# Kernel optimization log

Measured on AMD Instinct MI355X. Metric: run time of the kernel, lower is better.

The kernel has to match this reference:

```python
import jax, jax.numpy as jnp
import numpy as np

N = 50000        # n_nodes
E = 1_600_000    # n_edges (before self-loops)
D_IN, HID, HEADS, D_OUT = 32, 64, 4, 32
NEG_SLOPE = 0.2  # PyG GATConv default leaky_relu slope


def setup_inputs() -> dict:
    key = jax.random.key(0)
    ks = jax.random.split(key, 10)
    x = jax.random.normal(ks[0], (N, D_IN), jnp.float32)
    edge_index = jax.random.randint(ks[1], (2, E), 0, N, dtype=jnp.int64)
    s = 0.1
    W_gcn = jax.random.normal(ks[2], (D_IN, HID), jnp.float32) * s
    b_gcn = jnp.zeros((HID,), jnp.float32)
    W_gat = jax.random.normal(ks[3], (HID, HEADS * HID), jnp.float32) * s
    att_src = jax.random.normal(ks[4], (HEADS, HID), jnp.float32) * s
    att_dst = jax.random.normal(ks[5], (HEADS, HID), jnp.float32) * s
    b_gat = jnp.zeros((HEADS * HID,), jnp.float32)
    W_fc = jax.random.normal(ks[6], (HEADS * HID, D_OUT), jnp.float32) * s
    b_fc = jnp.zeros((D_OUT,), jnp.float32)
    return dict(x=x, edge_index=edge_index, W_gcn=W_gcn, b_gcn=b_gcn,
                W_gat=W_gat, att_src=att_src, att_dst=att_dst, b_gat=b_gat,
                W_fc=W_fc, b_fc=b_fc)


def _add_self_loops(edge_index, n):
    loop = jnp.arange(n, dtype=edge_index.dtype)
    src = jnp.concatenate([edge_index[0], loop])
    dst = jnp.concatenate([edge_index[1], loop])
    return src, dst


def _gcn(x, src, dst, W, b):
    h = x @ W                                               # (N, HID)
    deg = jax.ops.segment_sum(jnp.ones_like(src, jnp.float32), dst, N)
    dinv = jnp.where(deg > 0, jax.lax.rsqrt(deg), 0.0)
    norm = dinv[src] * dinv[dst]                            # (E+N,)
    out = jax.ops.segment_sum(h[src] * norm[:, None], dst, N)
    return out + b


def _gat(x, src, dst, W, att_src, att_dst, b):
    h = (x @ W).reshape(N, HEADS, HID)                      # (N, H, C)
    a_s = jnp.einsum('nhc,hc->nh', h, att_src)              # (N, H)
    a_d = jnp.einsum('nhc,hc->nh', h, att_dst)
    e = jax.nn.leaky_relu(a_s[src] + a_d[dst], NEG_SLOPE)   # (E+N, H)
    # softmax over incoming edges per destination node
    m = jax.ops.segment_max(e, dst, N)                      # every dst has a self-loop
    w = jnp.exp(e - m[dst])
    denom = jax.ops.segment_sum(w, dst, N)
    alpha = w / denom[dst]                                  # (E+N, H)
    out = jax.ops.segment_sum(h[src] * alpha[:, :, None], dst, N)
    return out.reshape(N, HEADS * HID) + b


def reference(x, edge_index, W_gcn, b_gcn, W_gat, att_src, att_dst, b_gat, W_fc, b_fc):
    src, dst = _add_self_loops(edge_index, N)
    h = jax.nn.relu(_gcn(x, src, dst, W_gcn, b_gcn))        # dropout: eval mode (identity)
    h = jax.nn.relu(_gat(h, src, dst, W_gat, att_src, att_dst, b_gat))
    return h @ W_fc + b_fc
```

## Files before the change

### kernel.cpp

```cpp
#include <hip/hip_runtime.h>
#include <hip/hip_bf16.h>
#include <hip/hip_fp16.h>
#include <math.h>

#define N_NODES 50000
#define N_EDGES 1600000
#define D_IN    32
#define HID     64
#define HEADS   4
#define D_OUT   32
#define NEG_SLOPE 0.2f
#define NTILES 3125

#define CQ 64

#define NBKT 196
#define NBLK_A 391
#define TILE_A 4096
#define GH (NBKT * NBLK_A)
#define NSB 300
#define CAP 10240

typedef _Float16 half8 __attribute__((ext_vector_type(8)));
typedef float    f32x4 __attribute__((ext_vector_type(4)));
typedef float    f32x2 __attribute__((ext_vector_type(2)));

__global__ __launch_bounds__(256) void histA(const int* __restrict__ edge,
                                             int* __restrict__ ghist) {
    __shared__ int hist[4][NBKT];
    int t = threadIdx.x, wv = t >> 6;
    for (int i = t; i < 4 * NBKT; i += 256) ((int*)hist)[i] = 0;
    __syncthreads();
    int base = blockIdx.x * TILE_A;
#pragma unroll
    for (int k = 0; k < 16; k++) {
        int i = base + k * 256 + t;
        if (i < N_EDGES) atomicAdd(&hist[wv][edge[N_EDGES + i] >> 8], 1);
    }
    __syncthreads();
    for (int b = t; b < NBKT; b += 256)
        ghist[b * NBLK_A + blockIdx.x] = hist[0][b] + hist[1][b] + hist[2][b] + hist[3][b];
}

__global__ __launch_bounds__(256) void scanB1(const int* __restrict__ g,
                                              int* __restrict__ bsum) {
    int t = threadIdx.x;
    int i = blockIdx.x * 256 + t;
    int v = (i < GH) ? g[i] : 0;
#pragma unroll
    for (int off = 32; off; off >>= 1) v += __shfl_xor(v, off);
    __shared__ int ws[4];
    if ((t & 63) == 0) ws[t >> 6] = v;
    __syncthreads();
    if (t == 0) bsum[blockIdx.x] = ws[0] + ws[1] + ws[2] + ws[3];
}

__global__ __launch_bounds__(320) void scanB2_attvec(int* __restrict__ bsum,
                                                     const float* __restrict__ W,
                                                     const float* __restrict__ att_s,
                                                     const float* __restrict__ att_d,
                                                     float* __restrict__ vsrc,
                                                     float* __restrict__ vdst) {
    int t = threadIdx.x, lane = t & 63, wv = t >> 6;
    if (blockIdx.x == 0) {
        int v = (t < NSB) ? bsum[t] : 0;
        int inc = v;
#pragma unroll
        for (int d = 1; d < 64; d <<= 1) {
            int u = __shfl_up(inc, d);
            if (lane >= d) inc += u;
        }
        __shared__ int ws[5];
        if (lane == 63) ws[wv] = inc;
        __syncthreads();
        int add = 0;
#pragma unroll
        for (int j = 0; j < 5; j++) if (j < wv) add += ws[j];
        if (t < NSB) bsum[t] = add + inc - v;
    } else if (t < 256) {
        int h = t >> 6, k = t & 63;
        float s_ = 0.f, d_ = 0.f;
#pragma unroll 8
        for (int c = 0; c < 64; c++) {
            float w = W[k * 256 + h * 64 + c];
            s_ += w * att_s[h * 64 + c];
            d_ += w * att_d[h * 64 + c];
        }
        vsrc[h * 64 + k] = s_;
        vdst[h * 64 + k] = d_;
    }
}

__global__ __launch_bounds__(256) void scanB3(int* __restrict__ g,
                                              const int* __restrict__ bsum) {
    int t = threadIdx.x, lane = t & 63, wv = t >> 6;
    int i = blockIdx.x * 256 + t;
    int v = (i < GH) ? g[i] : 0;
    int inc = v;
#pragma unroll
    for (int d = 1; d < 64; d <<= 1) {
        int u = __shfl_up(inc, d);
        if (lane >= d) inc += u;
    }
    __shared__ int ws[4];
    if (lane == 63) ws[wv] = inc;
    __syncthreads();
    int add = 0;
#pragma unroll
    for (int j = 0; j < 4; j++) if (j < wv) add += ws[j];
    if (i < GH) g[i] = bsum[blockIdx.x] + add + inc - v;
}

__global__ __launch_bounds__(256) void scatterC(const int* __restrict__ edge,
                                                const int* __restrict__ ghist,
                                                unsigned* __restrict__ tmp) {
    __shared__ int cur[NBKT];
    int t = threadIdx.x;
    if (t < NBKT) cur[t] = ghist[t * NBLK_A + blockIdx.x];
    __syncthreads();
    int base = blockIdx.x * TILE_A;
#pragma unroll
    for (int k = 0; k < 16; k++) {
        int i = base + k * 256 + t;
        if (i < N_EDGES) {
            int s = edge[i], d = edge[N_EDGES + i];
            int pos = atomicAdd(&cur[d >> 8], 1);
            tmp[pos] = ((unsigned)d << 16) | (unsigned)s;
        }
    }
}

__global__ __launch_bounds__(256) void sortD(const unsigned* __restrict__ tmp,
                                             const int* __restrict__ ghist,
                                             unsigned short* __restrict__ colidx,
                                             int* __restrict__ rowptr,
                                             float* __restrict__ dinv) {
    __shared__ unsigned char  dl8[CAP];
    __shared__ unsigned short s16[CAP];
    __shared__ unsigned short o16[CAP];
    __shared__ int hist[4][256];
    __shared__ int excl[256];
    __shared__ int wsum[4];
    int t = threadIdx.x, lane = t & 63, wv = t >> 6;
    int b = blockIdx.x;
    int lo = ghist[b * NBLK_A];
    int hi = (b < NBKT - 1) ? ghist[(b + 1) * NBLK_A] : N_EDGES;
    int size = hi - lo;
    if (size > CAP) size = CAP;
    for (int i = t; i < 4 * 256; i += 256) ((int*)hist)[i] = 0;
    __syncthreads();
    for (int i = t; i < size; i += 256) {
        unsigned key = tmp[lo + i];
        int dl = (key >> 16) & 255;
        dl8[i] = (unsigned char)dl;
        s16[i] = (unsigned short)(key & 0xFFFF);
        atomicAdd(&hist[wv][dl], 1);
    }
    __syncthreads();
    int h = hist[0][t] + hist[1][t] + hist[2][t] + hist[3][t];
    int inc = h;
#pragma unroll
    for (int d = 1; d < 64; d <<= 1) {
        int u = __shfl_up(inc, d);
        if (lane >= d) inc += u;
    }
    if (lane == 63) wsum[wv] = inc;
    __syncthreads();
    int add = 0;
#pragma unroll
    for (int j = 0; j < 4; j++) if (j < wv) add += wsum[j];
    int ex = inc - h + add;
    excl[t] = ex;
    int node = b * 256 + t;
    if (node < N_NODES) {
        rowptr[node] = lo + ex;
        dinv[node]   = rsqrtf((float)(h + 1));
    }
    if (b == NBKT - 1 && t == 0) rowptr[N_NODES] = N_EDGES;
    __syncthreads();
    for (int i = t; i < size; i += 256) {
        int pos = atomicAdd(&excl[dl8[i]], 1);
        o16[pos] = s16[i];
    }
    __syncthreads();
    for (int i = t; i < size; i += 256) colidx[lo + i] = o16[i];
}

__global__ __launch_bounds__(256) void gemm1(const float* __restrict__ x,
                                             const float* __restrict__ W,
                                             const float* __restrict__ dinv,
                                             __half* __restrict__ h,
                                             __half* __restrict__ h1) {
    __shared__ float Wl[D_IN * HID];
    int t = threadIdx.x;
    if (blockIdx.x == 0 && t < HID) {
        h [(size_t)N_NODES * HID + t] = __float2half(0.f);
        h1[(size_t)N_NODES * HID + t] = __float2half(0.f);
    }
    for (int i = t; i < D_IN * HID; i += 256) Wl[i] = W[i];
    __syncthreads();
    int c = t & 63, rw = t >> 6;
    int r0 = blockIdx.x * 32;
#pragma unroll
    for (int rr = 0; rr < 8; rr++) {
        int r = r0 + rr * 4 + rw;
        if (r >= N_NODES) break;
        const float4* xr4 = (const float4*)(x + r * D_IN);
        float acc = 0.f;
#pragma unroll
        for (int k4 = 0; k4 < D_IN / 4; k4++) {
            float4 xv = xr4[k4];
            int k = k4 * 4;
            acc += xv.x * Wl[(k+0)*HID + c] + xv.y * Wl[(k+1)*HID + c]
                 + xv.z * Wl[(k+2)*HID + c] + xv.w * Wl[(k+3)*HID + c];
        }
        h[r * HID + c] = __float2half(acc * dinv[r]);
    }
}

__global__ __launch_bounds__(256, 8) void gcn_agg(const __half* __restrict__ h,
                                               const int* __restrict__ rowptr,
                                               const unsigned short* __restrict__ colidx,
                                               const float* __restrict__ dinv,
                                               const float* __restrict__ b,
                                               const float* __restrict__ vsrc,
                                               const float* __restrict__ vdst,
                                               __half* __restrict__ h1,
                                               float* __restrict__ as_o,
                                               float* __restrict__ ad_o) {
    __shared__ int sbuf[4][4][CQ + 1];
    int lane = threadIdx.x & 63, wv = threadIdx.x >> 6;
    int quarter = lane >> 4, ql = lane & 15;
    int n = blockIdx.x * 16 + wv * 4 + quarter;
    int rp = rowptr[n], re = rowptr[n + 1];
    int deg = re - rp;
    int dm = deg;
    dm = max(dm, __shfl_xor(dm, 16));
    dm = max(dm, __shfl_xor(dm, 32));
    f32x2 a01 = {0.f, 0.f}, a23 = {0.f, 0.f};
    const __half* hp = h + ql * 4;
    int* sq = sbuf[wv][quarter];
    for (int cb = 0; cb < dm; cb += CQ) {
        int m  = min(CQ, max(deg - cb, 0));
        int mm = min(CQ, dm - cb);
        int mm8 = (mm + 7) & ~7;
        for (int j = ql; j < m; j += 16)
            sq[j] = (int)colidx[rp + cb + j] * HID;
        for (int j = m + ql; j < mm8; j += 16)
            sq[j] = N_NODES * HID;
        for (int i0 = 0; i0 < mm8; i0 += 8) {
            float2 raw[8];
#pragma unroll
            for (int k = 0; k < 8; k++)
                raw[k] = *(const float2*)(hp + sq[i0 + k]);
#pragma unroll
            for (int k = 0; k < 8; k++) {
                __half2 g0 = __builtin_bit_cast(__half2, raw[k].x);
                __half2 g1 = __builtin_bit_cast(__half2, raw[k].y);
                float2 f0 = __half22float2(g0), f1 = __half22float2(g1);
                a01.x += f0.x; a01.y += f0.y;
                a23.x += f1.x; a23.y += f1.y;
            }
        }
    }
    {
        float2 raw = *(const float2*)(hp + n * HID);
        __half2 g0 = __builtin_bit_cast(__half2, raw.x);
        __half2 g1 = __builtin_bit_cast(__half2, raw.y);
        float2 f0 = __half22float2(g0), f1 = __half22float2(g1);
        a01.x += f0.x; a01.y += f0.y;
        a23.x += f1.x; a23.y += f1.y;
    }
    float dn = dinv[n];
    const float4 bb = *(const float4*)&b[ql * 4];
    float v0 = fmaxf(a01.x * dn + bb.x, 0.f);
    float v1 = fmaxf(a01.y * dn + bb.y, 0.f);
    float v2 = fmaxf(a23.x * dn + bb.z, 0.f);
    float v3 = fmaxf(a23.y * dn + bb.w, 0.f);
    __half2* op = (__half2*)&h1[n * HID + ql * 4];
    op[0] = __floats2half2_rn(v0, v1);
    op[1] = __floats2half2_rn(v2, v3);
#pragma unroll
    for (int hh = 0; hh < 4; hh++) {
        float4 vsp = *(const float4*)&vsrc[hh * 64 + ql * 4];
        float4 vdp = *(const float4*)&vdst[hh * 64 + ql * 4];
        float vs = v0 * vsp.x + v1 * vsp.y + v2 * vsp.z + v3 * vsp.w;
        float vd = v0 * vdp.x + v1 * vdp.y + v2 * vdp.z + v3 * vdp.w;
#pragma unroll
        for (int off = 8; off > 0; off >>= 1) {
            vs += __shfl_xor(vs, off);
            vd += __shfl_xor(vd, off);
        }
        if (ql == 0) {
            as_o[n * 4 + hh] = vs;
            ad_o[n * 4 + hh] = vd;
        }
    }
}

__global__ __launch_bounds__(256, 8) void gat_agg(const __half* __restrict__ h1,
                                               const int* __restrict__ rowptr,
                                               const unsigned short* __restrict__ colidx,
                                               const float* __restrict__ a_s,
                                               const float* __restrict__ a_d,
                                               __half* __restrict__ u) {
    __shared__ float4 wbuf[4][4][CQ + 1];
    __shared__ int    sbuf[4][4][CQ + 1];
    int lane = threadIdx.x & 63, wv = threadIdx.x >> 6;
    int quarter = lane >> 4, ql = lane & 15;
    int n = blockIdx.x * 16 + wv * 4 + quarter;
    int rp = rowptr[n], re = rowptr[n + 1];
    int deg = re - rp;
    int dm = deg;
    dm = max(dm, __shfl_xor(dm, 16));
    dm = max(dm, __shfl_xor(dm, 32));
    float4 ad4 = *(const float4*)&a_d[n * 4];

    float dnx = 0.f, dny = 0.f, dnz = 0.f, dnw = 0.f;
    f32x2 acc[4][2];
#pragma unroll
    for (int hh = 0; hh < 4; hh++) { acc[hh][0] = (f32x2){0.f,0.f}; acc[hh][1] = (f32x2){0.f,0.f}; }
    const __half* hp = h1 + ql * 4;
    int*    sq = sbuf[wv][quarter];
    float4* wq = wbuf[wv][quarter];
    for (int cb = 0; cb < dm; cb += CQ) {
        int m  = min(CQ, max(deg - cb, 0));
        int mm = min(CQ, dm - cb);
        int mm8 = (mm + 7) & ~7;
        for (int j = ql; j < m; j += 16) {
            int s = colidx[rp + cb + j];
            float4 a = *(const float4*)&a_s[s * 4];
            float vx = a.x + ad4.x; vx = fmaxf(vx, NEG_SLOPE * vx);
            float vy = a.y + ad4.y; vy = fmaxf(vy, NEG_SLOPE * vy);
            float vz = a.z + ad4.z; vz = fmaxf(vz, NEG_SLOPE * vz);
            float vw = a.w + ad4.w; vw = fmaxf(vw, NEG_SLOPE * vw);
            float wx = __expf(vx), wy = __expf(vy);
            float wz = __expf(vz), ww = __expf(vw);
            dnx += wx; dny += wy; dnz += wz; dnw += ww;
            sq[j] = s * HID;
            wq[j] = make_float4(wx, wy, wz, ww);
        }
        for (int j = m + ql; j < mm8; j += 16) {
            sq[j] = N_NODES * HID;
            wq[j] = make_float4(0.f, 0.f, 0.f, 0.f);
        }
        for (int i0 = 0; i0 < mm8; i0 += 8) {
            float2 raw[8];
#pragma unroll
            for (int k = 0; k < 8; k++)
                raw[k] = *(const float2*)(hp + sq[i0 + k]);
#pragma unroll
            for (int k = 0; k < 8; k++) {
                float4 w4 = wq[i0 + k];
                __half2 g0 = __builtin_bit_cast(__half2, raw[k].x);
                __half2 g1 = __builtin_bit_cast(__half2, raw[k].y);
                float2 t0 = __half22float2(g0), t1 = __half22float2(g1);
                f32x2 f0 = {t0.x, t0.y}, f1 = {t1.x, t1.y};
                f32x2 wx2 = {w4.x, w4.x}, wy2 = {w4.y, w4.y};
                f32x2 wz2 = {w4.z, w4.z}, ww2 = {w4.w, w4.w};
                acc[0][0] += wx2 * f0; acc[0][1] += wx2 * f1;
                acc[1][0] += wy2 * f0; acc[1][1] += wy2 * f1;
                acc[2][0] += wz2 * f0; acc[2][1] += wz2 * f1;
                acc[3][0] += ww2 * f0; acc[3][1] += ww2 * f1;
            }
        }
    }
#pragma unroll
    for (int off = 8; off > 0; off >>= 1) {
        dnx += __shfl_xor(dnx, off);
        dny += __shfl_xor(dny, off);
        dnz += __shfl_xor(dnz, off);
        dnw += __shfl_xor(dnw, off);
    }
    float4 asn = *(const float4*)&a_s[n * 4];
    float sx = asn.x + ad4.x; sx = fmaxf(sx, NEG_SLOPE * sx);
    float sy = asn.y + ad4.y; sy = fmaxf(sy, NEG_SLOPE * sy);
    float sz = asn.z + ad4.z; sz = fmaxf(sz, NEG_SLOPE * sz);
    float sw = asn.w + ad4.w; sw = fmaxf(sw, NEG_SLOPE * sw);
    float wsx = __expf(sx), wsy = __expf(sy);
    float wsz = __expf(sz), wsw = __expf(sw);
    dnx += wsx; dny += wsy; dnz += wsz; dnw += wsw;
    {
        float2 raw = *(const float2*)(hp + n * HID);
        __half2 g0 = __builtin_bit_cast(__half2, raw.x);
        __half2 g1 = __builtin_bit_cast(__half2, raw.y);
        float2 t0 = __half22float2(g0), t1 = __half22float2(g1);
        acc[0][0].x += wsx * t0.x; acc[0][0].y += wsx * t0.y; acc[0][1].x += wsx * t1.x; acc[0][1].y += wsx * t1.y;
        acc[1][0].x += wsy * t0.x; acc[1][0].y += wsy * t0.y; acc[1][1].x += wsy * t1.x; acc[1][1].y += wsy * t1.y;
        acc[2][0].x += wsz * t0.x; acc[2][0].y += wsz * t0.y; acc[2][1].x += wsz * t1.x; acc[2][1].y += wsz * t1.y;
        acc[3][0].x += wsw * t0.x; acc[3][0].y += wsw * t0.y; acc[3][1].x += wsw * t1.x; acc[3][1].y += wsw * t1.y;
    }
    float r4[4] = {1.f / dnx, 1.f / dny, 1.f / dnz, 1.f / dnw};
    __half* up = u + n * 256 + ql * 4;
#pragma unroll
    for (int hh = 0; hh < 4; hh++) {
        __half2* op = (__half2*)&up[hh * 64];
        op[0] = __floats2half2_rn(acc[hh][0].x * r4[hh], acc[hh][0].y * r4[hh]);
        op[1] = __floats2half2_rn(acc[hh][1].x * r4[hh], acc[hh][1].y * r4[hh]);
    }
}

__global__ __launch_bounds__(256) void gemm2b(const __half* __restrict__ u,
                                              const float* __restrict__ W,
                                              const float* __restrict__ b,
                                              __half* __restrict__ h2) {
    int lane = threadIdx.x & 63, hd = threadIdx.x >> 6;
    int quad = lane >> 4, l16 = lane & 15;
    half8 Bf[4][2];
#pragma unroll
    for (int nt = 0; nt < 4; nt++)
#pragma unroll
        for (int kc = 0; kc < 2; kc++) {
            const float* wp = W + (kc * 32 + quad * 8) * 256 + hd * 64 + nt * 16 + l16;
#pragma unroll
            for (int j = 0; j < 8; j++)
                Bf[nt][kc][j] = (_Float16)wp[j * 256];
        }
    float bb[4];
#pragma unroll
    for (int nt = 0; nt < 4; nt++) bb[nt] = b[hd * 64 + nt * 16 + l16];

    int rt0 = blockIdx.x * 5;
#pragma unroll
    for (int i = 0; i < 5; i++) {
        int rt = rt0 + i;
        const __half* up = u + ((size_t)(rt * 16 + l16)) * 256 + hd * 64 + quad * 8;
        half8 A0 = *(const half8*)(const void*)up;
        half8 A1 = *(const half8*)(const void*)(up + 32);
        f32x4 acc[4];
#pragma unroll
        for (int nt = 0; nt < 4; nt++) {
            acc[nt] = (f32x4){0.f, 0.f, 0.f, 0.f};
            acc[nt] = __builtin_amdgcn_mfma_f32_16x16x32_f16(A0, Bf[nt][0], acc[nt], 0, 0, 0);
            acc[nt] = __builtin_amdgcn_mfma_f32_16x16x32_f16(A1, Bf[nt][1], acc[nt], 0, 0, 0);
        }
#pragma unroll
        for (int nt = 0; nt < 4; nt++) {
            int col = hd * 64 + nt * 16 + l16;
#pragma unroll
            for (int reg = 0; reg < 4; reg++) {
                int row = rt * 16 + quad * 4 + reg;
                h2[(size_t)row * 256 + col] = __float2half(fmaxf(acc[nt][reg] + bb[nt], 0.f));
            }
        }
    }
}

__global__ __launch_bounds__(256) void gemm3(const __half* __restrict__ h2,
                                             const float* __restrict__ W,
                                             const float* __restrict__ b,
                                             float* __restrict__ out) {
    int lane = threadIdx.x & 63, wv = threadIdx.x >> 6;
    int quad = lane >> 4, l16 = lane & 15;
    half8 Bf[2][8];
#pragma unroll
    for (int nt = 0; nt < 2; nt++)
#pragma unroll
        for (int kc = 0; kc < 8; kc++) {
            const float* wp = W + (kc * 32 + quad * 8) * 32 + nt * 16 + l16;
#pragma unroll
            for (int j = 0; j < 8; j++)
                Bf[nt][kc][j] = (_Float16)wp[j * 32];
        }
    float bb0 = b[l16], bb1 = b[16 + l16];

    for (int tile = blockIdx.x * 4 + wv; tile < NTILES; tile += gridDim.x * 4) {
        const __half* hp = h2 + (size_t)(tile * 16 + l16) * 256 + quad * 8;
        f32x4 acc0 = {0.f, 0.f, 0.f, 0.f};
        f32x4 acc1 = {0.f, 0.f, 0.f, 0.f};
#pragma unroll
        for (int kc = 0; kc < 8; kc++) {
            half8 A = *(const half8*)(const void*)(hp + kc * 32);
            acc0 = __builtin_amdgcn_mfma_f32_16x16x32_f16(A, Bf[0][kc], acc0, 0, 0, 0);
            acc1 = __builtin_amdgcn_mfma_f32_16x16x32_f16(A, Bf[1][kc], acc1, 0, 0, 0);
        }
#pragma unroll
        for (int reg = 0; reg < 4; reg++) {
            int row = tile * 16 + quad * 4 + reg;
            out[row * 32 + l16]      = acc0[reg] + bb0;
            out[row * 32 + 16 + l16] = acc1[reg] + bb1;
        }
    }
}

extern "C" void kernel_launch(void* const* d_in, const int* in_sizes, int n_in,
                              void* d_out, int out_size, void* d_ws, size_t ws_size,
                              hipStream_t stream) {
    const float* x      = (const float*)d_in[0];
    const int*   edge   = (const int*)  d_in[1];
    const float* W_gcn  = (const float*)d_in[2];
    const float* b_gcn  = (const float*)d_in[3];
    const float* W_gat  = (const float*)d_in[4];
    const float* att_s  = (const float*)d_in[5];
    const float* att_d  = (const float*)d_in[6];
    const float* b_gat  = (const float*)d_in[7];
    const float* W_fc   = (const float*)d_in[8];
    const float* b_fc   = (const float*)d_in[9];
    float* out = (float*)d_out;

    char* p = (char*)d_ws;
    auto alloc = [&](size_t bytes) {
        char* q = p;
        p += (bytes + 255) & ~(size_t)255;
        return q;
    };
    __half* h     = (__half*)alloc((size_t)(N_NODES + 1) * HID * 2);
    __half* h1    = (__half*)alloc((size_t)(N_NODES + 1) * HID * 2);
    __half* u     = (__half*)alloc((size_t)N_NODES * 256 * 2);
    __half* h2    = (__half*)alloc((size_t)N_NODES * 256 * 2);
    float* as_a   = (float*)alloc((size_t)N_NODES * 4 * 4);
    float* ad_a   = (float*)alloc((size_t)N_NODES * 4 * 4);
    float* dinv   = (float*)alloc((size_t)N_NODES * 4);
    int*   rowptr = (int*)  alloc((size_t)(N_NODES + 1) * 4);
    unsigned short* colidx = (unsigned short*)alloc((size_t)N_EDGES * 2);
    int*   ghist  = (int*)  alloc((size_t)GH * 4);
    int*   bsum   = (int*)  alloc((size_t)NSB * 4);
    unsigned* tmp = (unsigned*)alloc((size_t)N_EDGES * 4);
    float* vsrc   = (float*)alloc((size_t)HEADS * HID * 4);
    float* vdst   = (float*)alloc((size_t)HEADS * HID * 4);

    histA        <<<NBLK_A, 256, 0, stream>>>(edge, ghist);
    scanB1       <<<NSB, 256, 0, stream>>>(ghist, bsum);
    scanB2_attvec<<<2, 320, 0, stream>>>(bsum, W_gat, att_s, att_d, vsrc, vdst);
    scanB3       <<<NSB, 256, 0, stream>>>(ghist, bsum);
    scatterC     <<<NBLK_A, 256, 0, stream>>>(edge, ghist, tmp);
    sortD        <<<NBKT, 256, 0, stream>>>(tmp, ghist, colidx, rowptr, dinv);

    gemm1   <<<(N_NODES + 31) / 32, 256, 0, stream>>>(x, W_gcn, dinv, h, h1);
    gcn_agg <<<(N_NODES + 15) / 16, 256, 0, stream>>>(h, rowptr, colidx, dinv, b_gcn,
                                                      vsrc, vdst, h1, as_a, ad_a);

    gat_agg <<<(N_NODES + 15) / 16, 256, 0, stream>>>(h1, rowptr, colidx, as_a, ad_a, u);
    gemm2b  <<<625, 256, 0, stream>>>(u, W_gat, b_gat, h2);

    gemm3   <<<256, 256, 0, stream>>>(h2, W_fc, b_fc, out);
}
```

Baseline: 227.7 us.

## Process 8 nodes per wavefront with 16-byte gathers in GCN/GAT aggregation

Both aggregation kernels now assign 8 lanes per destination node instead of 16, so each lane gathers 8 fp16 features with a single 16-byte load, and each block covers 32 nodes. Bounds guards are added because 50000 is not a multiple of 32. The GAT neighbor chunk size is cut to 32 to keep shared memory in check, and the occupancy hint in launch_bounds is removed. This halves the number of gather instructions per edge and widens each load, at the cost of more registers per lane and more divergence across the 8 nodes in a wavefront.

```diff
diff --git a/kernel.cpp b/kernel.cpp
--- a/kernel.cpp
+++ b/kernel.cpp
@@ -12,7 +12,8 @@
 #define NEG_SLOPE 0.2f
 #define NTILES 3125
 
-#define CQ 64
+#define CQG 64
+#define CQA 32
 
 #define NBKT 196
 #define NBLK_A 391
@@ -218,7 +219,7 @@
     }
 }
 
-__global__ __launch_bounds__(256, 8) void gcn_agg(const __half* __restrict__ h,
+__global__ __launch_bounds__(256) void gcn_agg(const __half* __restrict__ h,
                                                const int* __restrict__ rowptr,
                                                const unsigned short* __restrict__ colidx,
                                                const float* __restrict__ dinv,
@@ -228,106 +229,134 @@
                                                __half* __restrict__ h1,
                                                float* __restrict__ as_o,
                                                float* __restrict__ ad_o) {
-    __shared__ int sbuf[4][4][CQ + 1];
+    __shared__ int sbuf[4][8][CQG + 1];
     int lane = threadIdx.x & 63, wv = threadIdx.x >> 6;
-    int quarter = lane >> 4, ql = lane & 15;
-    int n = blockIdx.x * 16 + wv * 4 + quarter;
-    int rp = rowptr[n], re = rowptr[n + 1];
-    int deg = re - rp;
+    int oct = lane >> 3, ol = lane & 7;
+    int n = blockIdx.x * 32 + wv * 8 + oct;
+    int nn = min(n, N_NODES - 1);
+    int rp = rowptr[nn], re = rowptr[nn + 1];
+    int deg = (n < N_NODES) ? (re - rp) : 0;
     int dm = deg;
+    dm = max(dm, __shfl_xor(dm, 8));
     dm = max(dm, __shfl_xor(dm, 16));
     dm = max(dm, __shfl_xor(dm, 32));
-    f32x2 a01 = {0.f, 0.f}, a23 = {0.f, 0.f};
-    const __half* hp = h + ql * 4;
-    int* sq = sbuf[wv][quarter];
-    for (int cb = 0; cb < dm; cb += CQ) {
-        int m  = min(CQ, max(deg - cb, 0));
-        int mm = min(CQ, dm - cb);
+    f32x4 a0 = {0.f,0.f,0.f,0.f}, a1 = {0.f,0.f,0.f,0.f};
+    const __half* hp = h + ol * 8;
+    int* sq = sbuf[wv][oct];
+    for (int cb = 0; cb < dm; cb += CQG) {
+        int m  = min(CQG, max(deg - cb, 0));
+        int mm = min(CQG, dm - cb);
         int mm8 = (mm + 7) & ~7;
-        for (int j = ql; j < m; j += 16)
+        for (int j = ol; j < m; j += 8)
             sq[j] = (int)colidx[rp + cb + j] * HID;
-        for (int j = m + ql; j < mm8; j += 16)
+        for (int j = m + ol; j < mm8; j += 8)
             sq[j] = N_NODES * HID;
         for (int i0 = 0; i0 < mm8; i0 += 8) {
-            float2 raw[8];
+            float4 raw[8];
 #pragma unroll
             for (int k = 0; k < 8; k++)
-                raw[k] = *(const float2*)(hp + sq[i0 + k]);
+                raw[k] = *(const float4*)(hp + sq[i0 + k]);
 #pragma unroll
             for (int k = 0; k < 8; k++) {
                 __half2 g0 = __builtin_bit_cast(__half2, raw[k].x);
                 __half2 g1 = __builtin_bit_cast(__half2, raw[k].y);
+                __half2 g2 = __builtin_bit_cast(__half2, raw[k].z);
+                __half2 g3 = __builtin_bit_cast(__half2, raw[k].w);
                 float2 f0 = __half22float2(g0), f1 = __half22float2(g1);
-                a01.x += f0.x; a01.y += f0.y;
-                a23.x += f1.x; a23.y += f1.y;
+                float2 f2 = __half22float2(g2), f3 = __half22float2(g3);
+                a0.x += f0.x; a0.y += f0.y; a0.z += f1.x; a0.w += f1.y;
+                a1.x += f2.x; a1.y += f2.y; a1.z += f3.x; a1.w += f3.y;
             }
         }
     }
     {
-        float2 raw = *(const float2*)(hp + n * HID);
+        float4 raw = *(const float4*)(hp + nn * HID);
         __half2 g0 = __builtin_bit_cast(__half2, raw.x);
         __half2 g1 = __builtin_bit_cast(__half2, raw.y);
+        __half2 g2 = __builtin_bit_cast(__half2, raw.z);
+        __half2 g3 = __builtin_bit_cast(__half2, raw.w);
         float2 f0 = __half22float2(g0), f1 = __half22float2(g1);
-        a01.x += f0.x; a01.y += f0.y;
-        a23.x += f1.x; a23.y += f1.y;
-    }
-    float dn = dinv[n];
-    const float4 bb = *(const float4*)&b[ql * 4];
-    float v0 = fmaxf(a01.x * dn + bb.x, 0.f);
-    float v1 = fmaxf(a01.y * dn + bb.y, 0.f);
-    float v2 = fmaxf(a23.x * dn + bb.z, 0.f);
-    float v3 = fmaxf(a23.y * dn + bb.w, 0.f);
-    __half2* op = (__half2*)&h1[n * HID + ql * 4];
-    op[0] = __floats2half2_rn(v0, v1);
-    op[1] = __floats2half2_rn(v2, v3);
+        float2 f2 = __half22float2(g2), f3 = __half22float2(g3);
+        a0.x += f0.x; a0.y += f0.y; a0.z += f1.x; a0.w += f1.y;
+        a1.x += f2.x; a1.y += f2.y; a1.z += f3.x; a1.w += f3.y;
+    }
+    float dn = dinv[nn];
+    const float4 bb0 = *(const float4*)&b[ol * 8];
+    const float4 bb1 = *(const float4*)&b[ol * 8 + 4];
+    float v0 = fmaxf(a0.x * dn + bb0.x, 0.f);
+    float v1 = fmaxf(a0.y * dn + bb0.y, 0.f);
+    float v2 = fmaxf(a0.z * dn + bb0.z, 0.f);
+    float v3 = fmaxf(a0.w * dn + bb0.w, 0.f);
+    float v4 = fmaxf(a1.x * dn + bb1.x, 0.f);
+    float v5 = fmaxf(a1.y * dn + bb1.y, 0.f);
+    float v6 = fmaxf(a1.z * dn + bb1.z, 0.f);
+    float v7 = fmaxf(a1.w * dn + bb1.w, 0.f);
+    if (n < N_NODES) {
+        __half2 p0 = __floats2half2_rn(v0, v1);
+        __half2 p1 = __floats2half2_rn(v2, v3);
+        __half2 p2 = __floats2half2_rn(v4, v5);
+        __half2 p3 = __floats2half2_rn(v6, v7);
+        float4 pk;
+        pk.x = __builtin_bit_cast(float, p0);
+        pk.y = __builtin_bit_cast(float, p1);
+        pk.z = __builtin_bit_cast(float, p2);
+        pk.w = __builtin_bit_cast(float, p3);
+        *(float4*)&h1[n * HID + ol * 8] = pk;
+    }
 #pragma unroll
     for (int hh = 0; hh < 4; hh++) {
-        float4 vsp = *(const float4*)&vsrc[hh * 64 + ql * 4];
-        float4 vdp = *(const float4*)&vdst[hh * 64 + ql * 4];
-        float vs = v0 * vsp.x + v1 * vsp.y + v2 * vsp.z + v3 * vsp.w;
-        float vd = v0 * vdp.x + v1 * vdp.y + v2 * vdp.z + v3 * vdp.w;
-#pragma unroll
-        for (int off = 8; off > 0; off >>= 1) {
+        const float4 s0 = *(const float4*)&vsrc[hh * 64 + ol * 8];
+        const float4 s1 = *(const float4*)&vsrc[hh * 64 + ol * 8 + 4];
+        const float4 d0 = *(const float4*)&vdst[hh * 64 + ol * 8];
+        const float4 d1 = *(const float4*)&vdst[hh * 64 + ol * 8 + 4];
+        float vs = v0*s0.x + v1*s0.y + v2*s0.z + v3*s0.w
+                 + v4*s1.x + v5*s1.y + v6*s1.z + v7*s1.w;
+        float vd = v0*d0.x + v1*d0.y + v2*d0.z + v3*d0.w
+                 + v4*d1.x + v5*d1.y + v6*d1.z + v7*d1.w;
+#pragma unroll
+        for (int off = 4; off > 0; off >>= 1) {
             vs += __shfl_xor(vs, off);
             vd += __shfl_xor(vd, off);
         }
-        if (ql == 0) {
+        if (ol == 0 && n < N_NODES) {
             as_o[n * 4 + hh] = vs;
             ad_o[n * 4 + hh] = vd;
         }
     }
 }
 
-__global__ __launch_bounds__(256, 8) void gat_agg(const __half* __restrict__ h1,
+__global__ __launch_bounds__(256) void gat_agg(const __half* __restrict__ h1,
                                                const int* __restrict__ rowptr,
                                                const unsigned short* __restrict__ colidx,
                                                const float* __restrict__ a_s,
                                                const float* __restrict__ a_d,
                                                __half* __restrict__ u) {
-    __shared__ float4 wbuf[4][4][CQ + 1];
-    __shared__ int    sbuf[4][4][CQ + 1];
+    __shared__ float4 wbuf[4][8][CQA + 1];
+    __shared__ int    sbuf[4][8][CQA + 1];
     int lane = threadIdx.x & 63, wv = threadIdx.x >> 6;
-    int quarter = lane >> 4, ql = lane & 15;
-    int n = blockIdx.x * 16 + wv * 4 + quarter;
-    int rp = rowptr[n], re = rowptr[n + 1];
-    int deg = re - rp;
+    int oct = lane >> 3, ol = lane & 7;
+    int n = blockIdx.x * 32 + wv * 8 + oct;
+    int nn = min(n, N_NODES - 1);
+    int rp = rowptr[nn], re = rowptr[nn + 1];
+    int deg = (n < N_NODES) ? (re - rp) : 0;
     int dm = deg;
+    dm = max(dm, __shfl_xor(dm, 8));
     dm = max(dm, __shfl_xor(dm, 16));
     dm = max(dm, __shfl_xor(dm, 32));
-    float4 ad4 = *(const float4*)&a_d[n * 4];
+    float4 ad4 = *(const float4*)&a_d[nn * 4];
 
     float dnx = 0.f, dny = 0.f, dnz = 0.f, dnw = 0.f;
-    f32x2 acc[4][2];
-#pragma unroll
-    for (int hh = 0; hh < 4; hh++) { acc[hh][0] = (f32x2){0.f,0.f}; acc[hh][1] = (f32x2){0.f,0.f}; }
-    const __half* hp = h1 + ql * 4;
-    int*    sq = sbuf[wv][quarter];
-    float4* wq = wbuf[wv][quarter];
-    for (int cb = 0; cb < dm; cb += CQ) {
-        int m  = min(CQ, max(deg - cb, 0));
-        int mm = min(CQ, dm - cb);
+    f32x4 accA[4], accB[4];
+#pragma unroll
+    for (int hh = 0; hh < 4; hh++) { accA[hh] = (f32x4){0.f,0.f,0.f,0.f}; accB[hh] = (f32x4){0.f,0.f,0.f,0.f}; }
+    const __half* hp = h1 + ol * 8;
+    int*    sq = sbuf[wv][oct];
+    float4* wq = wbuf[wv][oct];
+    for (int cb = 0; cb < dm; cb += CQA) {
+        int m  = min(CQA, max(deg - cb, 0));
+        int mm = min(CQA, dm - cb);
         int mm8 = (mm + 7) & ~7;
-        for (int j = ql; j < m; j += 16) {
+        for (int j = ol; j < m; j += 8) {
             int s = colidx[rp + cb + j];
             float4 a = *(const float4*)&a_s[s * 4];
             float vx = a.x + ad4.x; vx = fmaxf(vx, NEG_SLOPE * vx);
@@ -340,39 +369,45 @@
             sq[j] = s * HID;
             wq[j] = make_float4(wx, wy, wz, ww);
         }
-        for (int j = m + ql; j < mm8; j += 16) {
+        for (int j = m + ol; j < mm8; j += 8) {
             sq[j] = N_NODES * HID;
             wq[j] = make_float4(0.f, 0.f, 0.f, 0.f);
         }
         for (int i0 = 0; i0 < mm8; i0 += 8) {
-            float2 raw[8];
+            float4 raw[8];
 #pragma unroll
             for (int k = 0; k < 8; k++)
-                raw[k] = *(const float2*)(hp + sq[i0 + k]);
+                raw[k] = *(const float4*)(hp + sq[i0 + k]);
 #pragma unroll
             for (int k = 0; k < 8; k++) {
                 float4 w4 = wq[i0 + k];
                 __half2 g0 = __builtin_bit_cast(__half2, raw[k].x);
                 __half2 g1 = __builtin_bit_cast(__half2, raw[k].y);
-                float2 t0 = __half22float2(g0), t1 = __half22float2(g1);
-                f32x2 f0 = {t0.x, t0.y}, f1 = {t1.x, t1.y};
-                f32x2 wx2 = {w4.x, w4.x}, wy2 = {w4.y, w4.y};
-                f32x2 wz2 = {w4.z, w4.z}, ww2 = {w4.w, w4.w};
-                acc[0][0] += wx2 * f0; acc[0][1] += wx2 * f1;
-                acc[1][0] += wy2 * f0; acc[1][1] += wy2 * f1;
-                acc[2][0] += wz2 * f0; acc[2][1] += wz2 * f1;
-                acc[3][0] += ww2 * f0; acc[3][1] += ww2 * f1;
+                __half2 g2 = __builtin_bit_cast(__half2, raw[k].z);
+                __half2 g3 = __builtin_bit_cast(__half2, raw[k].w);
+                float2 f0 = __half22float2(g0), f1 = __half22float2(g1);
+                float2 f2 = __half22float2(g2), f3 = __half22float2(g3);
+                f32x4 flo = {f0.x, f0.y, f1.x, f1.y};
+                f32x4 fhi = {f2.x, f2.y, f3.x, f3.y};
+                f32x4 wxv = {w4.x, w4.x, w4.x, w4.x};
+                f32x4 wyv = {w4.y, w4.y, w4.y, w4.y};
+                f32x4 wzv = {w4.z, w4.z, w4.z, w4.z};
+                f32x4 wwv = {w4.w, w4.w, w4.w, w4.w};
+                accA[0] += wxv * flo; accB[0] += wxv * fhi;
+                accA[1] += wyv * flo; accB[1] += wyv * fhi;
+                accA[2] += wzv * flo; accB[2] += wzv * fhi;
+                accA[3] += wwv * flo; accB[3] += wwv * fhi;
             }
         }
     }
 #pragma unroll
-    for (int off = 8; off > 0; off >>= 1) {
+    for (int off = 4; off > 0; off >>= 1) {
         dnx += __shfl_xor(dnx, off);
         dny += __shfl_xor(dny, off);
         dnz += __shfl_xor(dnz, off);
         dnw += __shfl_xor(dnw, off);
     }
-    float4 asn = *(const float4*)&a_s[n * 4];
+    float4 asn = *(const float4*)&a_s[nn * 4];
     float sx = asn.x + ad4.x; sx = fmaxf(sx, NEG_SLOPE * sx);
     float sy = asn.y + ad4.y; sy = fmaxf(sy, NEG_SLOPE * sy);
     float sz = asn.z + ad4.z; sz = fmaxf(sz, NEG_SLOPE * sz);
@@ -381,22 +416,37 @@
     float wsz = __expf(sz), wsw = __expf(sw);
     dnx += wsx; dny += wsy; dnz += wsz; dnw += wsw;
     {
-        float2 raw = *(const float2*)(hp + n * HID);
+        float4 raw = *(const float4*)(hp + nn * HID);
         __half2 g0 = __builtin_bit_cast(__half2, raw.x);
         __half2 g1 = __builtin_bit_cast(__half2, raw.y);
-        float2 t0 = __half22float2(g0), t1 = __half22float2(g1);
-        acc[0][0].x += wsx * t0.x; acc[0][0].y += wsx * t0.y; acc[0][1].x += wsx * t1.x; acc[0][1].y += wsx * t1.y;
-        acc[1][0].x += wsy * t0.x; acc[1][0].y += wsy * t0.y; acc[1][1].x += wsy * t1.x; acc[1][1].y += wsy * t1.y;
-        acc[2][0].x += wsz * t0.x; acc[2][0].y += wsz * t0.y; acc[2][1].x += wsz * t1.x; acc[2][1].y += wsz * t1.y;
-        acc[3][0].x += wsw * t0.x; acc[3][0].y += wsw * t0.y; acc[3][1].x += wsw * t1.x; acc[3][1].y += wsw * t1.y;
-    }
-    float r4[4] = {1.f / dnx, 1.f / dny, 1.f / dnz, 1.f / dnw};
-    __half* up = u + n * 256 + ql * 4;
-#pragma unroll
-    for (int hh = 0; hh < 4; hh++) {
-        __half2* op = (__half2*)&up[hh * 64];
-        op[0] = __floats2half2_rn(acc[hh][0].x * r4[hh], acc[hh][0].y * r4[hh]);
-        op[1] = __floats2half2_rn(acc[hh][1].x * r4[hh], acc[hh][1].y * r4[hh]);
+        __half2 g2 = __builtin_bit_cast(__half2, raw.z);
+        __half2 g3 = __builtin_bit_cast(__half2, raw.w);
+        float2 f0 = __half22float2(g0), f1 = __half22float2(g1);
+        float2 f2 = __half22float2(g2), f3 = __half22float2(g3);
+        f32x4 flo = {f0.x, f0.y, f1.x, f1.y};
+        f32x4 fhi = {f2.x, f2.y, f3.x, f3.y};
+        accA[0] += (f32x4){wsx,wsx,wsx,wsx} * flo; accB[0] += (f32x4){wsx,wsx,wsx,wsx} * fhi;
+        accA[1] += (f32x4){wsy,wsy,wsy,wsy} * flo; accB[1] += (f32x4){wsy,wsy,wsy,wsy} * fhi;
+        accA[2] += (f32x4){wsz,wsz,wsz,wsz} * flo; accB[2] += (f32x4){wsz,wsz,wsz,wsz} * fhi;
+        accA[3] += (f32x4){wsw,wsw,wsw,wsw} * flo; accB[3] += (f32x4){wsw,wsw,wsw,wsw} * fhi;
+    }
+    if (n < N_NODES) {
+        float r4[4] = {1.f / dnx, 1.f / dny, 1.f / dnz, 1.f / dnw};
+        __half* up = u + (size_t)n * 256 + ol * 8;
+#pragma unroll
+        for (int hh = 0; hh < 4; hh++) {
+            float r = r4[hh];
+            __half2 p0 = __floats2half2_rn(accA[hh].x * r, accA[hh].y * r);
+            __half2 p1 = __floats2half2_rn(accA[hh].z * r, accA[hh].w * r);
+            __half2 p2 = __floats2half2_rn(accB[hh].x * r, accB[hh].y * r);
+            __half2 p3 = __floats2half2_rn(accB[hh].z * r, accB[hh].w * r);
+            float4 pk;
+            pk.x = __builtin_bit_cast(float, p0);
+            pk.y = __builtin_bit_cast(float, p1);
+            pk.z = __builtin_bit_cast(float, p2);
+            pk.w = __builtin_bit_cast(float, p3);
+            *(float4*)&up[hh * 64] = pk;
+        }
     }
 }
 
@@ -527,10 +577,10 @@
     sortD        <<<NBKT, 256, 0, stream>>>(tmp, ghist, colidx, rowptr, dinv);
 
     gemm1   <<<(N_NODES + 31) / 32, 256, 0, stream>>>(x, W_gcn, dinv, h, h1);
-    gcn_agg <<<(N_NODES + 15) / 16, 256, 0, stream>>>(h, rowptr, colidx, dinv, b_gcn,
+    gcn_agg <<<(N_NODES + 31) / 32, 256, 0, stream>>>(h, rowptr, colidx, dinv, b_gcn,
                                                       vsrc, vdst, h1, as_a, ad_a);
 
-    gat_agg <<<(N_NODES + 15) / 16, 256, 0, stream>>>(h1, rowptr, colidx, as_a, ad_a, u);
+    gat_agg <<<(N_NODES + 31) / 32, 256, 0, stream>>>(h1, rowptr, colidx, as_a, ad_a, u);
     gemm2b  <<<625, 256, 0, stream>>>(u, W_gat, b_gat, h2);
 
     gemm3   <<<256, 256, 0, stream>>>(h2, W_fc, b_fc, out);
```

After: 221.9 us. 1.03x faster.
